# Kernel tuning notes

Measured on AMD Instinct MI355X. Metric: run time of the kernel, lower is better.

The kernel has to match this reference:

```python
import jax, jax.numpy as jnp
import numpy as np

N = 50000      # nodes
E = 800000     # edges (avg degree 16)
F_IN = 512
HID = 128
OUT = 40


def setup_inputs() -> dict:
    key = jax.random.key(0)
    ks = jax.random.split(key, 6)
    x = jax.random.normal(ks[0], (N, F_IN), dtype=jnp.float32)
    edge_index = jax.random.randint(ks[1], (2, E), 0, N, dtype=jnp.int64)
    edge_weight = jax.random.uniform(ks[2], (E,), dtype=jnp.float32)
    # Glorot-ish init for the two GCNConv weight matrices
    W1 = jax.random.normal(ks[3], (F_IN, HID), dtype=jnp.float32) * (1.0 / np.sqrt(F_IN))
    b1 = jnp.zeros((HID,), dtype=jnp.float32)
    W2 = jax.random.normal(ks[4], (HID, OUT), dtype=jnp.float32) * (1.0 / np.sqrt(HID))
    b2 = jnp.zeros((OUT,), dtype=jnp.float32)
    return {"x": x, "edge_index": edge_index, "edge_weight": edge_weight,
            "W1": W1, "b1": b1, "W2": W2, "b2": b2}


def gcn_layer(x, edge_index, edge_weight, W, b):
    """PyG GCNConv (normalize=True, add_self_loops=True):
    out = D^{-1/2} (A + I) D^{-1/2} (x @ W) + b, with weighted edges."""
    n = x.shape[0]
    h = x @ W  # [n, F_out] dense transform before aggregation
    sl = jnp.arange(n)
    row = jnp.concatenate([edge_index[0], sl])   # source nodes
    col = jnp.concatenate([edge_index[1], sl])   # target nodes
    w = jnp.concatenate([edge_weight, jnp.ones((n,), x.dtype)])  # self-loop weight 1
    deg = jax.ops.segment_sum(w, col, num_segments=n)            # in-degree (weighted)
    dinv = jnp.where(deg > 0, jax.lax.rsqrt(deg), 0.0)
    norm = dinv[row] * w * dinv[col]                             # per-edge coefficient
    # gather-source, scale, scatter-add into target
    out = jax.ops.segment_sum(h[row] * norm[:, None], col, num_segments=n)
    return out + b


def reference(x, edge_index, edge_weight, W1, b1, W2, b2):
    h = jax.nn.relu(gcn_layer(x, edge_index, edge_weight, W1, b1))
    # dropout is identity at inference (training=False)
    h = gcn_layer(h, edge_index, edge_weight, W2, b2)
    return jax.nn.log_softmax(h, axis=1)
```

## Files before the change

### kernel.cpp

```cpp
#include <hip/hip_runtime.h>
#include <math.h>

#define N_NODES 50000
#define F_IN    512
#define HID     128
#define OUT_C   40
#define NPAD    48
#define E_EDGES 800000
#define LDA 40
#define LDK 136
#define MAXDEG 64
#define ESTRIDE 48
#define G1B 391
#define DEGB 3125

typedef __attribute__((ext_vector_type(8))) short short8;
typedef __attribute__((ext_vector_type(4))) float f32x4;
typedef __attribute__((ext_vector_type(4))) unsigned uint4v;

__device__ __forceinline__ unsigned short f2bf(float f) {
    union { float f; unsigned u; } v; v.f = f;
    unsigned u = v.u + 0x7fffu + ((v.u >> 16) & 1u);
    return (unsigned short)(u >> 16);
}
__device__ __forceinline__ float bflo(unsigned u) { return __uint_as_float(u << 16); }
__device__ __forceinline__ float bfhi(unsigned u) { return __uint_as_float(u & 0xffff0000u); }
__device__ __forceinline__ unsigned cvtpk(float lo, float hi) {
    unsigned r;
    asm("v_cvt_pk_bf16_f32 %0, %1, %2" : "=v"(r) : "v"(lo), "v"(hi));
    return r;
}
__device__ __forceinline__ float pk2dinv(unsigned pk) {
    return rsqrtf(1.0f + (float)(pk & 0x03FFFFFFu) * (1.0f / 1048576.0f));
}


__global__ __launch_bounds__(256) void k_initwprep(const float* __restrict__ W1,
                                                   const float* __restrict__ W2,
                                                   unsigned short* __restrict__ W1bt,
                                                   unsigned short* __restrict__ W2bt,
                                                   unsigned* __restrict__ packed) {
    int idx = blockIdx.x * 256 + threadIdx.x;
    if (idx < N_NODES) packed[idx] = 0u;
    if (idx < F_IN * HID) {
        int k = idx & 511, n = idx >> 9;
        W1bt[(size_t)n * F_IN + k] = f2bf(W1[(size_t)k * HID + n]);
    } else if (idx < F_IN * HID + NPAD * HID) {
        int i2 = idx - F_IN * HID;
        int k = i2 & 127, n = i2 >> 7;
        W2bt[n * HID + k] = (n < OUT_C) ? f2bf(W2[(size_t)k * OUT_C + n]) : 0;
    }
}


__global__ __launch_bounds__(256) void k_g1deg(const float* __restrict__ X,
                                               const unsigned short* __restrict__ W1bt,
                                               unsigned short* __restrict__ Hb,
                                               const int* __restrict__ row,
                                               const int* __restrict__ col,
                                               const float* __restrict__ ew,
                                               unsigned* __restrict__ packed,
                                               unsigned* __restrict__ es) {
    const int tid = threadIdx.x;
    if (blockIdx.x >= G1B) {
        int e = (blockIdx.x - G1B) * 256 + tid;
        if (e < E_EDGES) {
            int c   = col[e];
            int r   = row[e];
            float w = ew[e];
            unsigned fx = (unsigned)(w * 1048576.0f);
            unsigned old = atomicAdd(&packed[c], (1u << 26) | fx);
            int rk = (int)(old >> 26);
            if (rk < ESTRIDE)
                es[(size_t)c * ESTRIDE + rk] = (unsigned)r | ((unsigned)f2bf(w) << 16);
        }
        return;
    }

    __shared__ __align__(16) unsigned short As[128 * LDA];
    __shared__ __align__(16) unsigned short Bs[128 * LDA];
    const int row0 = blockIdx.x * 128;
    const int lane = tid & 63;
    const int w    = tid >> 6;
    const int quad = lane >> 4;
    const int l16  = lane & 15;
    const int wm   = (w >> 1) * 64;
    const int wn   = (w & 1) * 64;

    f32x4 acc[4][4] = {};

    const int sr = tid >> 1;
    const int kg = (tid & 1) * 16;
    int arow = row0 + sr;
    if (arow >= N_NODES) arow = N_NODES - 1;
    const float*          xp = X + (size_t)arow * F_IN + kg;
    const unsigned short* bp = W1bt + (size_t)sr * F_IN + kg;
    unsigned short* asw = &As[sr * LDA + kg];
    unsigned short* bsw = &Bs[sr * LDA + kg];

    float4 xa = *(const float4*)(xp);
    float4 xb = *(const float4*)(xp + 4);
    float4 xc = *(const float4*)(xp + 8);
    float4 xd = *(const float4*)(xp + 12);
    short8 wa = *(const short8*)(bp);
    short8 wb = *(const short8*)(bp + 8);

    for (int k0 = 0; k0 < F_IN; k0 += 32) {
        uint4v pa, pb;
        pa[0] = cvtpk(xa.x, xa.y); pa[1] = cvtpk(xa.z, xa.w);
        pa[2] = cvtpk(xb.x, xb.y); pa[3] = cvtpk(xb.z, xb.w);
        pb[0] = cvtpk(xc.x, xc.y); pb[1] = cvtpk(xc.z, xc.w);
        pb[2] = cvtpk(xd.x, xd.y); pb[3] = cvtpk(xd.z, xd.w);
        short8 cwa = wa, cwb = wb;

        if (k0 + 32 < F_IN) {
            xa = *(const float4*)(xp + k0 + 32);
            xb = *(const float4*)(xp + k0 + 36);
            xc = *(const float4*)(xp + k0 + 40);
            xd = *(const float4*)(xp + k0 + 44);
            wa = *(const short8*)(bp + k0 + 32);
            wb = *(const short8*)(bp + k0 + 40);
        }

        *(uint4v*)(asw)      = pa;
        *(uint4v*)(asw + 8)  = pb;
        *(short8*)(bsw)      = cwa;
        *(short8*)(bsw + 8)  = cwb;
        asm volatile("s_waitcnt lgkmcnt(0)" ::: "memory");
        __builtin_amdgcn_s_barrier();
        asm volatile("" ::: "memory");

        short8 af[4], bf[4];
#pragma unroll
        for (int i = 0; i < 4; i++)
            af[i] = *(const short8*)&As[(wm + i * 16 + l16) * LDA + quad * 8];
#pragma unroll
        for (int j = 0; j < 4; j++)
            bf[j] = *(const short8*)&Bs[(wn + j * 16 + l16) * LDA + quad * 8];
#pragma unroll
        for (int i = 0; i < 4; i++)
#pragma unroll
            for (int j = 0; j < 4; j++)
                acc[i][j] = __builtin_amdgcn_mfma_f32_16x16x32_bf16(
                    af[i], bf[j], acc[i][j], 0, 0, 0);
        asm volatile("" ::: "memory");
        __builtin_amdgcn_s_barrier();
        asm volatile("" ::: "memory");
    }

#pragma unroll
    for (int i = 0; i < 4; i++) {
#pragma unroll
        for (int r = 0; r < 4; r++) {
            int grow = row0 + wm + i * 16 + quad * 4 + r;
            if (grow < N_NODES) {
#pragma unroll
                for (int j = 0; j < 4; j++) {
                    int gcol = wn + j * 16 + l16;
                    Hb[(size_t)grow * HID + gcol] = f2bf(acc[i][j][r]);
                }
            }
        }
    }
}


__global__ __launch_bounds__(256) void k_agg1(const unsigned* __restrict__ packed,
                                              const unsigned* __restrict__ es,
                                              const unsigned short* __restrict__ H1b,
                                              const float* __restrict__ b1,
                                              unsigned short* __restrict__ A1b) {
    __shared__ int2 sE[4][MAXDEG];
    const int tid  = threadIdx.x;
    const int wv   = tid >> 6;
    const int lane = tid & 63;
    const int node = blockIdx.x * 4 + wv;
    if (node >= N_NODES) return;
    const int q   = lane >> 4;
    const int l16 = lane & 15;

    const unsigned pkn = packed[node];
    const int   d  = (int)(pkn >> 26);
    const float di = pk2dinv(pkn);
    const size_t base = (size_t)node * ESTRIDE;
    int dl = (d < ESTRIDE) ? d : ESTRIDE;
    const int dp = (dl + 15) & ~15;
    for (int p = lane; p < dp; p += 64) {
        int2 t = make_int2(0, 0);
        if (p < dl) {
            unsigned u = es[base + p];
            float dv = pk2dinv(packed[u & 0xffffu]);
            t.x = (int)(u & 0xffffu);
            t.y = __float_as_int(bfhi(u) * dv);
        }
        sE[wv][p] = t;
    }

    const uint4 sv = *(const uint4*)&H1b[(size_t)node * HID + l16 * 8];
    float a[8];
    if (q == 0) {
        a[0] = di * bflo(sv.x); a[1] = di * bfhi(sv.x);
        a[2] = di * bflo(sv.y); a[3] = di * bfhi(sv.y);
        a[4] = di * bflo(sv.z); a[5] = di * bfhi(sv.z);
        a[6] = di * bflo(sv.w); a[7] = di * bfhi(sv.w);
    } else {
#pragma unroll
        for (int k = 0; k < 8; k++) a[k] = 0.0f;
    }

    for (int p = 0; p < dp; p += 16) {
        const int bs = p + q * 4;
        int s_[4]; float n_[4];
#pragma unroll
        for (int j = 0; j < 4; j++) {
            int2 t = sE[wv][bs + j];
            s_[j] = t.x; n_[j] = __int_as_float(t.y);
        }
        uint4 g[4];
#pragma unroll
        for (int j = 0; j < 4; j++)
            g[j] = *(const uint4*)&H1b[(size_t)s_[j] * HID + l16 * 8];
#pragma unroll
        for (int j = 0; j < 4; j++) {
            a[0] = fmaf(bflo(g[j].x), n_[j], a[0]);
            a[1] = fmaf(bfhi(g[j].x), n_[j], a[1]);
            a[2] = fmaf(bflo(g[j].y), n_[j], a[2]);
            a[3] = fmaf(bfhi(g[j].y), n_[j], a[3]);
            a[4] = fmaf(bflo(g[j].z), n_[j], a[4]);
            a[5] = fmaf(bfhi(g[j].z), n_[j], a[5]);
            a[6] = fmaf(bflo(g[j].w), n_[j], a[6]);
            a[7] = fmaf(bfhi(g[j].w), n_[j], a[7]);
        }
    }

#pragma unroll
    for (int k = 0; k < 8; k++) {
        a[k] += __shfl_xor(a[k], 16);
        a[k] += __shfl_xor(a[k], 32);
    }

    if (q == 0) {
        const float4 bv0 = *(const float4*)&b1[l16 * 8];
        const float4 bv1 = *(const float4*)&b1[l16 * 8 + 4];
        float r0 = fmaxf(fmaf(di, a[0], bv0.x), 0.0f);
        float r1 = fmaxf(fmaf(di, a[1], bv0.y), 0.0f);
        float r2 = fmaxf(fmaf(di, a[2], bv0.z), 0.0f);
        float r3 = fmaxf(fmaf(di, a[3], bv0.w), 0.0f);
        float r4 = fmaxf(fmaf(di, a[4], bv1.x), 0.0f);
        float r5 = fmaxf(fmaf(di, a[5], bv1.y), 0.0f);
        float r6 = fmaxf(fmaf(di, a[6], bv1.z), 0.0f);
        float r7 = fmaxf(fmaf(di, a[7], bv1.w), 0.0f);
        uint4 pk4;
        pk4.x = cvtpk(r0, r1);
        pk4.y = cvtpk(r2, r3);
        pk4.z = cvtpk(r4, r5);
        pk4.w = cvtpk(r6, r7);
        *(uint4*)&A1b[(size_t)node * HID + l16 * 8] = pk4;
    }
}


__global__ __launch_bounds__(256) void k_gemm2_mfma(const unsigned short* __restrict__ A1b,
                                                    const unsigned short* __restrict__ W2bt,
                                                    const unsigned* __restrict__ packed,
                                                    unsigned short* __restrict__ H2b) {
    __shared__ __align__(16) unsigned short As[128 * LDK];
    __shared__ __align__(16) unsigned short Bs[NPAD * LDK];
    const int tid  = threadIdx.x;
    const int row0 = blockIdx.x * 128;
    const int lane = tid & 63;
    const int w    = tid >> 6;
    const int quad = lane >> 4;
    const int l16  = lane & 15;

#pragma unroll
    for (int i = 0; i < 8; i++) {
        int id = tid + i * 256;
        int r = id >> 4, kc = (id & 15) * 8;
        int ar = row0 + r; if (ar >= N_NODES) ar = N_NODES - 1;
        *(short8*)&As[r * LDK + kc] = *(const short8*)&A1b[(size_t)ar * HID + kc];
    }
#pragma unroll
    for (int i = 0; i < 3; i++) {
        int id = tid + i * 256;
        int n = id >> 4, kc = (id & 15) * 8;
        *(short8*)&Bs[n * LDK + kc] = *(const short8*)&W2bt[n * HID + kc];
    }
    __syncthreads();

    f32x4 acc[2][3] = {};
    const int rbase = w * 32;
#pragma unroll
    for (int ks = 0; ks < 4; ks++) {
        const int k0 = ks * 32 + quad * 8;
        short8 af[2], bf[3];
#pragma unroll
        for (int i = 0; i < 2; i++)
            af[i] = *(const short8*)&As[(rbase + i * 16 + l16) * LDK + k0];
#pragma unroll
        for (int j = 0; j < 3; j++)
            bf[j] = *(const short8*)&Bs[(j * 16 + l16) * LDK + k0];
#pragma unroll
        for (int i = 0; i < 2; i++)
#pragma unroll
            for (int j = 0; j < 3; j++)
                acc[i][j] = __builtin_amdgcn_mfma_f32_16x16x32_bf16(
                    af[i], bf[j], acc[i][j], 0, 0, 0);
    }

#pragma unroll
    for (int i = 0; i < 2; i++) {
#pragma unroll
        for (int r = 0; r < 4; r++) {
            int grow = row0 + rbase + i * 16 + quad * 4 + r;
            if (grow < N_NODES) {
                float dv = pk2dinv(packed[grow]);
#pragma unroll
                for (int j = 0; j < 3; j++)
                    H2b[(size_t)grow * NPAD + j * 16 + l16] = f2bf(dv * acc[i][j][r]);
            }
        }
    }
}


__global__ __launch_bounds__(256) void k_agg2_lsm(const unsigned* __restrict__ packed,
                                                  const unsigned* __restrict__ es,
                                                  const unsigned short* __restrict__ H2b,
                                                  const float* __restrict__ b2,
                                                  float* __restrict__ out) {
    __shared__ int2 sE[4][MAXDEG];
    const int tid  = threadIdx.x;
    const int wv   = tid >> 6;
    const int lane = tid & 63;
    const int node = blockIdx.x * 4 + wv;
    if (node >= N_NODES) return;
    const int q   = lane >> 4;
    const int l16 = lane & 15;
    const bool act = (l16 < 10);

    const unsigned pkn = packed[node];
    const int   d  = (int)(pkn >> 26);
    const float di = pk2dinv(pkn);
    const size_t base = (size_t)node * ESTRIDE;
    int dl = (d < ESTRIDE) ? d : ESTRIDE;
    const int dp = (dl + 15) & ~15;
    for (int p = lane; p < dp; p += 64) {
        int2 t = make_int2(0, 0);
        if (p < dl) {
            unsigned u = es[base + p];
            t.x = (int)(u & 0xffffu);
            t.y = __float_as_int(bfhi(u));
        }
        sE[wv][p] = t;
    }

    float a[4] = {0.0f, 0.0f, 0.0f, 0.0f};
    if (q == 0 && act) {
        uint2 sv = *(const uint2*)&H2b[(size_t)node * NPAD + 4 * l16];
        a[0] = bflo(sv.x); a[1] = bfhi(sv.x);
        a[2] = bflo(sv.y); a[3] = bfhi(sv.y);
    }

    for (int p = 0; p < dp; p += 16) {
        const int bs = p + q * 4;
        int s_[4]; float n_[4];
#pragma unroll
        for (int j = 0; j < 4; j++) {
            int2 t = sE[wv][bs + j];
            s_[j] = t.x; n_[j] = __int_as_float(t.y);
        }
        if (act) {
            uint2 g[4];
#pragma unroll
            for (int j = 0; j < 4; j++)
                g[j] = *(const uint2*)&H2b[(size_t)s_[j] * NPAD + 4 * l16];
#pragma unroll
            for (int j = 0; j < 4; j++) {
                a[0] = fmaf(bflo(g[j].x), n_[j], a[0]);
                a[1] = fmaf(bfhi(g[j].x), n_[j], a[1]);
                a[2] = fmaf(bflo(g[j].y), n_[j], a[2]);
                a[3] = fmaf(bfhi(g[j].y), n_[j], a[3]);
            }
        }
    }

#pragma unroll
    for (int k = 0; k < 4; k++) {
        a[k] += __shfl_xor(a[k], 16);
        a[k] += __shfl_xor(a[k], 32);
    }

    float v[4];
    float m = -INFINITY;
    if (act) {
        const float4 bv = *(const float4*)&b2[4 * l16];
        v[0] = fmaf(di, a[0], bv.x);
        v[1] = fmaf(di, a[1], bv.y);
        v[2] = fmaf(di, a[2], bv.z);
        v[3] = fmaf(di, a[3], bv.w);
        m = fmaxf(fmaxf(v[0], v[1]), fmaxf(v[2], v[3]));
    }
#pragma unroll
    for (int off = 8; off > 0; off >>= 1) m = fmaxf(m, __shfl_xor(m, off));
    float ex = 0.0f;
    if (act)
        ex = __expf(v[0] - m) + __expf(v[1] - m) + __expf(v[2] - m) + __expf(v[3] - m);
    float s = ex;
#pragma unroll
    for (int off = 8; off > 0; off >>= 1) s += __shfl_xor(s, off);
    if (q == 0 && act) {
        float lg = __logf(s);
        float4 o;
        o.x = v[0] - m - lg; o.y = v[1] - m - lg;
        o.z = v[2] - m - lg; o.w = v[3] - m - lg;
        *(float4*)&out[(size_t)node * OUT_C + 4 * l16] = o;
    }
}


extern "C" void kernel_launch(void* const* d_in, const int* in_sizes, int n_in,
                              void* d_out, int out_size, void* d_ws, size_t ws_size,
                              hipStream_t stream) {
    const float* x  = (const float*)d_in[0];
    const int*   ei = (const int*)d_in[1];
    const float* ew = (const float*)d_in[2];
    const float* W1 = (const float*)d_in[3];
    const float* b1 = (const float*)d_in[4];
    const float* W2 = (const float*)d_in[5];
    const float* b2 = (const float*)d_in[6];
    float* out = (float*)d_out;

    const int* row = ei;
    const int* col = ei + E_EDGES;

    float* ws = (float*)d_ws;
    unsigned* packed     = (unsigned*)ws;
    unsigned short* H1b  = (unsigned short*)(ws + 100000);
    unsigned short* H2b  = (unsigned short*)(ws + 100000);
    unsigned short* A1b  = (unsigned short*)(ws + 3300000);
    unsigned short* W1bt = (unsigned short*)(ws + 6500000);
    unsigned short* W2bt = (unsigned short*)(ws + 6532768);
    unsigned* es         = (unsigned*)(ws + 6535840);

    const int B = 256;

    k_initwprep<<<(F_IN * HID + NPAD * HID + B - 1) / B, B, 0, stream>>>(
        W1, W2, W1bt, W2bt, packed);

    k_g1deg<<<G1B + DEGB, B, 0, stream>>>(x, W1bt, H1b, row, col, ew, packed, es);

    k_agg1<<<(N_NODES + 3) / 4, B, 0, stream>>>(packed, es, H1b, b1, A1b);

    k_gemm2_mfma<<<(N_NODES + 127) / 128, B, 0, stream>>>(A1b, W2bt, packed, H2b);

    k_agg2_lsm<<<(N_NODES + 3) / 4, B, 0, stream>>>(packed, es, H2b, b2, out);
}
```

Before: 258.8 us.

## Unroll aggregation to fixed 32-edge chunk and put degree blocks first

Both aggregation kernels now always process the first 32 edge slots in one straight-line unrolled pass of 8 gathers per lane, padded with zero-weight entries. A 16-edge tail handles nodes with more than 32 edges. This replaces the variable-trip loop of 4 gathers per lane and raises memory-level parallelism. Padded slots gather node 0 at weight zero, which costs wasted loads for low-degree nodes. The fused GEMM/degree kernel also reorders its blocks so the degree-scatter blocks come first and the GEMM blocks after.

```diff
diff --git a/kernel.cpp b/kernel.cpp
--- a/kernel.cpp
+++ b/kernel.cpp
@@ -62,8 +62,8 @@
                                                unsigned* __restrict__ packed,
                                                unsigned* __restrict__ es) {
     const int tid = threadIdx.x;
-    if (blockIdx.x >= G1B) {
-        int e = (blockIdx.x - G1B) * 256 + tid;
+    if (blockIdx.x < DEGB) {
+        int e = blockIdx.x * 256 + tid;
         if (e < E_EDGES) {
             int c   = col[e];
             int r   = row[e];
@@ -79,7 +79,7 @@
 
     __shared__ __align__(16) unsigned short As[128 * LDA];
     __shared__ __align__(16) unsigned short Bs[128 * LDA];
-    const int row0 = blockIdx.x * 128;
+    const int row0 = (blockIdx.x - DEGB) * 128;
     const int lane = tid & 63;
     const int w    = tid >> 6;
     const int quad = lane >> 4;
@@ -184,8 +184,8 @@
     const float di = pk2dinv(pkn);
     const size_t base = (size_t)node * ESTRIDE;
     int dl = (d < ESTRIDE) ? d : ESTRIDE;
-    const int dp = (dl + 15) & ~15;
-    for (int p = lane; p < dp; p += 64) {
+    const int dps = (dl <= 32) ? 32 : 48;
+    for (int p = lane; p < dps; p += 64) {
         int2 t = make_int2(0, 0);
         if (p < dl) {
             unsigned u = es[base + p];
@@ -208,8 +208,32 @@
         for (int k = 0; k < 8; k++) a[k] = 0.0f;
     }
 
-    for (int p = 0; p < dp; p += 16) {
-        const int bs = p + q * 4;
+    {
+        const int bs = q * 8;
+        int s_[8]; float n_[8];
+#pragma unroll
+        for (int j = 0; j < 8; j++) {
+            int2 t = sE[wv][bs + j];
+            s_[j] = t.x; n_[j] = __int_as_float(t.y);
+        }
+        uint4 g[8];
+#pragma unroll
+        for (int j = 0; j < 8; j++)
+            g[j] = *(const uint4*)&H1b[(size_t)s_[j] * HID + l16 * 8];
+#pragma unroll
+        for (int j = 0; j < 8; j++) {
+            a[0] = fmaf(bflo(g[j].x), n_[j], a[0]);
+            a[1] = fmaf(bfhi(g[j].x), n_[j], a[1]);
+            a[2] = fmaf(bflo(g[j].y), n_[j], a[2]);
+            a[3] = fmaf(bfhi(g[j].y), n_[j], a[3]);
+            a[4] = fmaf(bflo(g[j].z), n_[j], a[4]);
+            a[5] = fmaf(bfhi(g[j].z), n_[j], a[5]);
+            a[6] = fmaf(bflo(g[j].w), n_[j], a[6]);
+            a[7] = fmaf(bfhi(g[j].w), n_[j], a[7]);
+        }
+    }
+    if (dl > 32) {
+        const int bs = 32 + q * 4;
         int s_[4]; float n_[4];
 #pragma unroll
         for (int j = 0; j < 4; j++) {
@@ -344,8 +368,8 @@
     const float di = pk2dinv(pkn);
     const size_t base = (size_t)node * ESTRIDE;
     int dl = (d < ESTRIDE) ? d : ESTRIDE;
-    const int dp = (dl + 15) & ~15;
-    for (int p = lane; p < dp; p += 64) {
+    const int dps = (dl <= 32) ? 32 : 48;
+    for (int p = lane; p < dps; p += 64) {
         int2 t = make_int2(0, 0);
         if (p < dl) {
             unsigned u = es[base + p];
@@ -362,8 +386,30 @@
         a[2] = bflo(sv.y); a[3] = bfhi(sv.y);
     }
 
-    for (int p = 0; p < dp; p += 16) {
-        const int bs = p + q * 4;
+    {
+        const int bs = q * 8;
+        int s_[8]; float n_[8];
+#pragma unroll
+        for (int j = 0; j < 8; j++) {
+            int2 t = sE[wv][bs + j];
+            s_[j] = t.x; n_[j] = __int_as_float(t.y);
+        }
+        if (act) {
+            uint2 g[8];
+#pragma unroll
+            for (int j = 0; j < 8; j++)
+                g[j] = *(const uint2*)&H2b[(size_t)s_[j] * NPAD + 4 * l16];
+#pragma unroll
+            for (int j = 0; j < 8; j++) {
+                a[0] = fmaf(bflo(g[j].x), n_[j], a[0]);
+                a[1] = fmaf(bfhi(g[j].x), n_[j], a[1]);
+                a[2] = fmaf(bflo(g[j].y), n_[j], a[2]);
+                a[3] = fmaf(bfhi(g[j].y), n_[j], a[3]);
+            }
+        }
+    }
+    if (dl > 32) {
+        const int bs = 32 + q * 4;
         int s_[4]; float n_[4];
 #pragma unroll
         for (int j = 0; j < 4; j++) {
```

Measured after the change: 297.3 us. +14.9%, slower.
